# Performance work log

Measured on AMD Instinct MI355X. Metric: run time of the kernel, lower is better.

## Reference

```python
import jax, jax.numpy as jnp
import numpy as np

C_S, C_Z, MAX_LEN, N_AA, L = 256, 128, 1024, 21, 512
LN_EPS = 1e-5


def setup_inputs() -> dict:
    key = jax.random.key(0)
    ks = jax.random.split(key, 12)
    inp = {
        "seq": jax.random.randint(ks[0], (L,), 0, N_AA),
        "chain_id_res": jax.random.randint(ks[1], (L,), 0, 2),
        "res_idx": jax.random.randint(ks[2], (L,), 0, L),
        # learned parameters
        "E_aa": jax.random.normal(ks[3], (N_AA, C_S), jnp.float32) * 0.02,
        "E_pos": jax.random.normal(ks[4], (MAX_LEN, C_S), jnp.float32) * 0.02,
        "E_chain": jax.random.normal(ks[5], (2, C_S), jnp.float32) * 0.02,
        "E_chainpair": jax.random.normal(ks[6], (4, C_Z), jnp.float32) * 0.02,
        "E_relpos": jax.random.normal(ks[7], (66, C_Z), jnp.float32) * 0.02,
        "W_pair": jax.random.normal(ks[8], (3 * C_S, C_Z), jnp.float32) / np.sqrt(3 * C_S),
        "b_pair": jnp.zeros((C_Z,), jnp.float32),
        "ln_w": jnp.ones((C_S,), jnp.float32),
        "ln_b": jnp.zeros((C_S,), jnp.float32),
    }
    return inp


def reference(seq, chain_id_res, res_idx, E_aa, E_pos, E_chain, E_chainpair,
              E_relpos, W_pair, b_pair, ln_w, ln_b):
    # single rep: sum of three embedding lookups -> [L, c_s]
    s = E_aa[seq] + E_pos[res_idx] + E_chain[chain_id_res]

    # LayerNorm over last dim
    mu = jnp.mean(s, axis=-1, keepdims=True)
    var = jnp.mean(jnp.square(s - mu), axis=-1, keepdims=True)
    u = (s - mu) * jax.lax.rsqrt(var + LN_EPS) * ln_w + ln_b  # [L, c_s]

    # pair_proj(cat(u_i, u_j, u_i*u_j)) decomposed: W = [W1; W2; W3]
    W1, W2, W3 = W_pair[:C_S], W_pair[C_S:2 * C_S], W_pair[2 * C_S:]
    zi = u @ W1                                   # [L, c_z] per-i term
    zj = u @ W2                                   # [L, c_z] per-j term
    zx = jnp.einsum('ic,jc,cz->ijz', u, u, W3)    # cross term (u_i*u_j) @ W3
    z = zi[:, None, :] + zj[None, :, :] + zx + b_pair  # [L, L, c_z]

    # chain-pair and relative-position embeddings
    chain_pair = chain_id_res[:, None] * 2 + chain_id_res[None, :]  # [L, L] in [0,3]
    same_chain = chain_id_res[:, None] == chain_id_res[None, :]
    diff = res_idx[:, None] - res_idx[None, :]
    clipped = jnp.clip(diff, -32, 32) + 32
    relpos = jnp.where(same_chain, clipped, 65)  # cross-chain bucket = 65

    z = z + E_chainpair[chain_pair] + E_relpos[relpos]
    return s, z
```

## Files before the change

kernel.cpp:

```cpp
#include <hip/hip_runtime.h>
#include <hip/hip_bf16.h>

#define L 512
#define CS 256
#define CZ 128
#define LN_EPS 1e-5f

typedef _Float16 f16_t;
typedef f16_t f16x8 __attribute__((ext_vector_type(8)));
typedef float f32x4 __attribute__((ext_vector_type(4)));

__global__ __launch_bounds__(256) void k_prep(
    const int* __restrict__ seq, const int* __restrict__ cid,
    const int* __restrict__ ridx,
    const float* __restrict__ Eaa, const float* __restrict__ Epos,
    const float* __restrict__ Ech, const float* __restrict__ lnw,
    const float* __restrict__ lnb, const float* __restrict__ Wp,
    const float* __restrict__ bp, const float* __restrict__ Ecp,
    const float* __restrict__ Erp,
    float* __restrict__ s_out, f16_t* __restrict__ u2,
    float* __restrict__ zrow, float* __restrict__ zcol,
    f16_t* __restrict__ w3c, float* __restrict__ tab)
{
    __shared__ float su[CS];
    __shared__ float red[8];
    const int i = blockIdx.x;
    const int c = threadIdx.x;

    if (i < 128) {
        w3c[(c >> 3) * (CZ * 8) + i * 8 + (c & 7)] = (f16_t)Wp[(2 * CS + c) * CZ + i];
    } else if (i < 128 + 264) {
        const int b2 = i - 128;
        if (c < CZ)
            tab[b2 * CZ + c] = Ecp[(b2 / 66) * CZ + c] + Erp[(b2 % 66) * CZ + c];
    }

    const int sq = seq[i], ri = ridx[i], ci = cid[i];
    const float v = Eaa[sq * CS + c] + Epos[ri * CS + c] + Ech[ci * CS + c];
    s_out[i * CS + c] = v;

    float s1 = v, s2 = v * v;
    #pragma unroll
    for (int o = 32; o > 0; o >>= 1) {
        s1 += __shfl_down(s1, o, 64);
        s2 += __shfl_down(s2, o, 64);
    }
    const int wv = c >> 6, lane = c & 63;
    if (lane == 0) { red[wv * 2] = s1; red[wv * 2 + 1] = s2; }
    __syncthreads();
    const float S  = red[0] + red[2] + red[4] + red[6];
    const float SS = red[1] + red[3] + red[5] + red[7];
    const float mu  = S * (1.0f / CS);
    const float var = SS * (1.0f / CS) - mu * mu;
    const float rs  = rsqrtf(var + LN_EPS);
    const float u   = (v - mu) * rs * lnw[c] + lnb[c];
    u2[(c >> 3) * (L * 8) + i * 8 + (c & 7)] = (f16_t)u;
    su[c] = u;
    __syncthreads();

    const int z = c & 127;
    const int half = c >> 7;
    const float* W = Wp + half * CS * CZ + z;
    float a0 = 0, a1 = 0, a2 = 0, a3 = 0;
    #pragma unroll 8
    for (int cc = 0; cc < CS; cc += 4) {
        a0 += su[cc + 0] * W[(cc + 0) * CZ];
        a1 += su[cc + 1] * W[(cc + 1) * CZ];
        a2 += su[cc + 2] * W[(cc + 2) * CZ];
        a3 += su[cc + 3] * W[(cc + 3) * CZ];
    }
    const float acc = (a0 + a1) + (a2 + a3);
    if (half) zcol[i * CZ + z] = acc;
    else      zrow[i * CZ + z] = acc + bp[z];
}

__global__ __launch_bounds__(512, 4) void k_pair(
    const f16_t* __restrict__ u2, const f16_t* __restrict__ w3c,
    const float* __restrict__ zrow, const float* __restrict__ zcol,
    const float* __restrict__ tab,
    const int* __restrict__ cid, const int* __restrict__ ridx,
    float* __restrict__ zout)
{
    __shared__ f16_t lds[(1024 + 256) * 8];
    f16x8* lj = (f16x8*)lds;
    f16x8* li = ((f16x8*)lds) + 1024;

    const int t = threadIdx.x;
    const int lane = t & 63, wave = t >> 6;
    const int m = lane & 15, q = lane >> 4;
    const int j0 = blockIdx.x * 32, i0 = blockIdx.y * 8;
    const int zseg = wave * 16;
    const int zq = zseg + q * 4;

    const f16x8* pu = (const f16x8*)u2;
    const f16x8* pw = (const f16x8*)w3c;

    if (t < 256) li[t] = pu[(t >> 3) * L + i0 + (t & 7)];
    #pragma unroll
    for (int rep = 0; rep < 2; ++rep) {
        const int un = rep * 512 + t;
        lj[un] = pu[(un >> 5) * L + j0 + (un & 31)];
    }

    f16x8 A[8];
    #pragma unroll
    for (int k32 = 0; k32 < 8; ++k32)
        A[k32] = pw[(k32 * 4 + q) * CZ + zseg + m];

    const int ja = j0 + m, jb = j0 + 16 + m;
    const int cja = cid[ja], rja = ridx[ja];
    const int cjb = cid[jb], rjb = ridx[jb];
    f32x4 ZCa = *(const f32x4*)&zcol[ja * CZ + zq];
    f32x4 ZCb = *(const f32x4*)&zcol[jb * CZ + zq];

    __syncthreads();

    #pragma unroll
    for (int ig = 0; ig < 4; ++ig) {
        const int i_0 = i0 + ig * 2, i_1 = i_0 + 1;

        const int ci0 = cid[i_0], ri0 = ridx[i_0];
        const int ci1 = cid[i_1], ri1 = ridx[i_1];
        int d;
        d = ri0 - rja; d = d < -32 ? -32 : (d > 32 ? 32 : d);
        const int x0a = ((ci0 * 2 + cja) * 66) + ((ci0 == cja) ? (d + 32) : 65);
        d = ri0 - rjb; d = d < -32 ? -32 : (d > 32 ? 32 : d);
        const int x0b = ((ci0 * 2 + cjb) * 66) + ((ci0 == cjb) ? (d + 32) : 65);
        d = ri1 - rja; d = d < -32 ? -32 : (d > 32 ? 32 : d);
        const int x1a = ((ci1 * 2 + cja) * 66) + ((ci1 == cja) ? (d + 32) : 65);
        d = ri1 - rjb; d = d < -32 ? -32 : (d > 32 ? 32 : d);
        const int x1b = ((ci1 * 2 + cjb) * 66) + ((ci1 == cjb) ? (d + 32) : 65);
        f32x4 zr0 = *(const f32x4*)&zrow[i_0 * CZ + zq];
        f32x4 zr1 = *(const f32x4*)&zrow[i_1 * CZ + zq];
        f32x4 t0a = *(const f32x4*)&tab[x0a * CZ + zq];
        f32x4 t0b = *(const f32x4*)&tab[x0b * CZ + zq];
        f32x4 t1a = *(const f32x4*)&tab[x1a * CZ + zq];
        f32x4 t1b = *(const f32x4*)&tab[x1b * CZ + zq];

        f32x4 a0a = {0,0,0,0}, a0b = {0,0,0,0};
        f32x4 a1a = {0,0,0,0}, a1b = {0,0,0,0};
        #pragma unroll
        for (int k32 = 0; k32 < 8; ++k32) {
            const int cb = k32 * 4 + q;
            f16x8 uja = lj[cb * 32 + m];
            f16x8 ujb = lj[cb * 32 + 16 + m];
            f16x8 ui0 = li[cb * 8 + ig * 2];
            f16x8 ui1 = li[cb * 8 + ig * 2 + 1];
            a0a = __builtin_amdgcn_mfma_f32_16x16x32_f16(A[k32], ui0 * uja, a0a, 0, 0, 0);
            a0b = __builtin_amdgcn_mfma_f32_16x16x32_f16(A[k32], ui0 * ujb, a0b, 0, 0, 0);
            a1a = __builtin_amdgcn_mfma_f32_16x16x32_f16(A[k32], ui1 * uja, a1a, 0, 0, 0);
            a1b = __builtin_amdgcn_mfma_f32_16x16x32_f16(A[k32], ui1 * ujb, a1b, 0, 0, 0);
        }

        float* r0 = zout + ((size_t)i_0 * L + j0 + m) * CZ + zq;
        float* r1 = zout + ((size_t)i_1 * L + j0 + m) * CZ + zq;
        f32x4 o;
        o = a0a + zr0 + ZCa + t0a; *(f32x4*)r0 = o;
        o = a0b + zr0 + ZCb + t0b; *(f32x4*)(r0 + 16 * CZ) = o;
        o = a1a + zr1 + ZCa + t1a; *(f32x4*)r1 = o;
        o = a1b + zr1 + ZCb + t1b; *(f32x4*)(r1 + 16 * CZ) = o;
    }
}

extern "C" void kernel_launch(void* const* d_in, const int* in_sizes, int n_in,
                              void* d_out, int out_size, void* d_ws, size_t ws_size,
                              hipStream_t stream) {
    const int*   seq  = (const int*)d_in[0];
    const int*   cid  = (const int*)d_in[1];
    const int*   ridx = (const int*)d_in[2];
    const float* Eaa  = (const float*)d_in[3];
    const float* Epos = (const float*)d_in[4];
    const float* Ech  = (const float*)d_in[5];
    const float* Ecp  = (const float*)d_in[6];
    const float* Erp  = (const float*)d_in[7];
    const float* Wp   = (const float*)d_in[8];
    const float* bp   = (const float*)d_in[9];
    const float* lnw  = (const float*)d_in[10];
    const float* lnb  = (const float*)d_in[11];

    float* out   = (float*)d_out;
    float* s_out = out;
    float* zout  = out + L * CS;

    char* ws = (char*)d_ws;
    f16_t* u2   = (f16_t*)ws;
    f16_t* w3c  = (f16_t*)(ws + 262144);
    float* zrow = (float*)(ws + 327680);
    float* zcol = (float*)(ws + 589824);
    float* tab  = (float*)(ws + 851968);

    hipLaunchKernelGGL(k_prep, dim3(L), dim3(256), 0, stream,
                       seq, cid, ridx, Eaa, Epos, Ech, lnw, lnb, Wp, bp,
                       Ecp, Erp, s_out, u2, zrow, zcol, w3c, tab);
    hipLaunchKernelGGL(k_pair, dim3(16, 64), dim3(512), 0, stream,
                       u2, w3c, zrow, zcol, tab, cid, ridx, zout);
}
```

Baseline: 173.0 us.

## Drop LDS staging in pair kernel and retile waves over z and i

Removes the shared-memory staging and the block barrier from the pair kernel. Each wave now loads its u_j fragments, two W3 fragments and per-i u vectors straight from global memory into registers. Blocks cover 16 j by 8 i, and each wave handles 32 z channels for 4 i rows, so the grid doubles along j. Occupancy launch bounds drop from 4 to 2 to allow more registers per thread. In exchange, global load traffic per block rises and fewer waves are resident, which could hurt latency hiding in a kernel dominated by output stores.

```diff
diff --git a/kernel.cpp b/kernel.cpp
--- a/kernel.cpp
+++ b/kernel.cpp
@@ -74,91 +74,84 @@
     else      zrow[i * CZ + z] = acc + bp[z];
 }
 
-__global__ __launch_bounds__(512, 4) void k_pair(
+__global__ __launch_bounds__(512, 2) void k_pair(
     const f16_t* __restrict__ u2, const f16_t* __restrict__ w3c,
     const float* __restrict__ zrow, const float* __restrict__ zcol,
     const float* __restrict__ tab,
     const int* __restrict__ cid, const int* __restrict__ ridx,
     float* __restrict__ zout)
 {
-    __shared__ f16_t lds[(1024 + 256) * 8];
-    f16x8* lj = (f16x8*)lds;
-    f16x8* li = ((f16x8*)lds) + 1024;
-
     const int t = threadIdx.x;
     const int lane = t & 63, wave = t >> 6;
     const int m = lane & 15, q = lane >> 4;
-    const int j0 = blockIdx.x * 32, i0 = blockIdx.y * 8;
-    const int zseg = wave * 16;
-    const int zq = zseg + q * 4;
+    const int j0 = blockIdx.x * 16, i0 = blockIdx.y * 8;
+    const int zsg = (wave & 3) * 32;
+    const int ibase = i0 + (wave >> 2) * 4;
+    const int zq0 = zsg + q * 4;
+    const int zq1 = zsg + 16 + q * 4;
 
     const f16x8* pu = (const f16x8*)u2;
     const f16x8* pw = (const f16x8*)w3c;
 
-    if (t < 256) li[t] = pu[(t >> 3) * L + i0 + (t & 7)];
+    f16x8 A0[8], A1[8], Uj[8];
     #pragma unroll
-    for (int rep = 0; rep < 2; ++rep) {
-        const int un = rep * 512 + t;
-        lj[un] = pu[(un >> 5) * L + j0 + (un & 31)];
+    for (int k32 = 0; k32 < 8; ++k32) {
+        const int cb = k32 * 4 + q;
+        A0[k32] = pw[cb * CZ + zsg + m];
+        A1[k32] = pw[cb * CZ + zsg + 16 + m];
+        Uj[k32] = pu[cb * L + j0 + m];
     }
+    const int jm = j0 + m;
+    const int cj = cid[jm], rj = ridx[jm];
+    const f32x4 ZC0 = *(const f32x4*)&zcol[jm * CZ + zq0];
+    const f32x4 ZC1 = *(const f32x4*)&zcol[jm * CZ + zq1];
 
-    f16x8 A[8];
-    #pragma unroll
-    for (int k32 = 0; k32 < 8; ++k32)
-        A[k32] = pw[(k32 * 4 + q) * CZ + zseg + m];
+    for (int ip = 0; ip < 2; ++ip) {
+        const int ia = ibase + ip * 2, ib = ia + 1;
 
-    const int ja = j0 + m, jb = j0 + 16 + m;
-    const int cja = cid[ja], rja = ridx[ja];
-    const int cjb = cid[jb], rjb = ridx[jb];
-    f32x4 ZCa = *(const f32x4*)&zcol[ja * CZ + zq];
-    f32x4 ZCb = *(const f32x4*)&zcol[jb * CZ + zq];
-
-    __syncthreads();
-
-    #pragma unroll
-    for (int ig = 0; ig < 4; ++ig) {
-        const int i_0 = i0 + ig * 2, i_1 = i_0 + 1;
-
-        const int ci0 = cid[i_0], ri0 = ridx[i_0];
-        const int ci1 = cid[i_1], ri1 = ridx[i_1];
-        int d;
-        d = ri0 - rja; d = d < -32 ? -32 : (d > 32 ? 32 : d);
-        const int x0a = ((ci0 * 2 + cja) * 66) + ((ci0 == cja) ? (d + 32) : 65);
-        d = ri0 - rjb; d = d < -32 ? -32 : (d > 32 ? 32 : d);
-        const int x0b = ((ci0 * 2 + cjb) * 66) + ((ci0 == cjb) ? (d + 32) : 65);
-        d = ri1 - rja; d = d < -32 ? -32 : (d > 32 ? 32 : d);
-        const int x1a = ((ci1 * 2 + cja) * 66) + ((ci1 == cja) ? (d + 32) : 65);
-        d = ri1 - rjb; d = d < -32 ? -32 : (d > 32 ? 32 : d);
-        const int x1b = ((ci1 * 2 + cjb) * 66) + ((ci1 == cjb) ? (d + 32) : 65);
-        f32x4 zr0 = *(const f32x4*)&zrow[i_0 * CZ + zq];
-        f32x4 zr1 = *(const f32x4*)&zrow[i_1 * CZ + zq];
-        f32x4 t0a = *(const f32x4*)&tab[x0a * CZ + zq];
-        f32x4 t0b = *(const f32x4*)&tab[x0b * CZ + zq];
-        f32x4 t1a = *(const f32x4*)&tab[x1a * CZ + zq];
-        f32x4 t1b = *(const f32x4*)&tab[x1b * CZ + zq];
-
-        f32x4 a0a = {0,0,0,0}, a0b = {0,0,0,0};
-        f32x4 a1a = {0,0,0,0}, a1b = {0,0,0,0};
+        f16x8 Ua[8], Ub[8];
         #pragma unroll
         for (int k32 = 0; k32 < 8; ++k32) {
             const int cb = k32 * 4 + q;
-            f16x8 uja = lj[cb * 32 + m];
-            f16x8 ujb = lj[cb * 32 + 16 + m];
-            f16x8 ui0 = li[cb * 8 + ig * 2];
-            f16x8 ui1 = li[cb * 8 + ig * 2 + 1];
-            a0a = __builtin_amdgcn_mfma_f32_16x16x32_f16(A[k32], ui0 * uja, a0a, 0, 0, 0);
-            a0b = __builtin_amdgcn_mfma_f32_16x16x32_f16(A[k32], ui0 * ujb, a0b, 0, 0, 0);
-            a1a = __builtin_amdgcn_mfma_f32_16x16x32_f16(A[k32], ui1 * uja, a1a, 0, 0, 0);
-            a1b = __builtin_amdgcn_mfma_f32_16x16x32_f16(A[k32], ui1 * ujb, a1b, 0, 0, 0);
+            Ua[k32] = pu[cb * L + ia];
+            Ub[k32] = pu[cb * L + ib];
         }
 
-        float* r0 = zout + ((size_t)i_0 * L + j0 + m) * CZ + zq;
-        float* r1 = zout + ((size_t)i_1 * L + j0 + m) * CZ + zq;
+        const int ca = cid[ia], ra = ridx[ia];
+        const int cb2 = cid[ib], rb2 = ridx[ib];
+        int d;
+        d = ra - rj;  d = d < -32 ? -32 : (d > 32 ? 32 : d);
+        const int xa = ((ca * 2 + cj) * 66) + ((ca == cj) ? (d + 32) : 65);
+        d = rb2 - rj; d = d < -32 ? -32 : (d > 32 ? 32 : d);
+        const int xb = ((cb2 * 2 + cj) * 66) + ((cb2 == cj) ? (d + 32) : 65);
+        f32x4 zra0 = *(const f32x4*)&zrow[ia * CZ + zq0];
+        f32x4 zra1 = *(const f32x4*)&zrow[ia * CZ + zq1];
+        f32x4 zrb0 = *(const f32x4*)&zrow[ib * CZ + zq0];
+        f32x4 zrb1 = *(const f32x4*)&zrow[ib * CZ + zq1];
+        f32x4 ta0 = *(const f32x4*)&tab[xa * CZ + zq0];
+        f32x4 ta1 = *(const f32x4*)&tab[xa * CZ + zq1];
+        f32x4 tb0 = *(const f32x4*)&tab[xb * CZ + zq0];
+        f32x4 tb1 = *(const f32x4*)&tab[xb * CZ + zq1];
+
+        f32x4 aa0 = {0,0,0,0}, aa1 = {0,0,0,0};
+        f32x4 ab0 = {0,0,0,0}, ab1 = {0,0,0,0};
+        #pragma unroll
+        for (int k32 = 0; k32 < 8; ++k32) {
+            const f16x8 Ba = Ua[k32] * Uj[k32];
+            const f16x8 Bb = Ub[k32] * Uj[k32];
+            aa0 = __builtin_amdgcn_mfma_f32_16x16x32_f16(A0[k32], Ba, aa0, 0, 0, 0);
+            aa1 = __builtin_amdgcn_mfma_f32_16x16x32_f16(A1[k32], Ba, aa1, 0, 0, 0);
+            ab0 = __builtin_amdgcn_mfma_f32_16x16x32_f16(A0[k32], Bb, ab0, 0, 0, 0);
+            ab1 = __builtin_amdgcn_mfma_f32_16x16x32_f16(A1[k32], Bb, ab1, 0, 0, 0);
+        }
+
+        float* r_a = zout + ((size_t)ia * L + jm) * CZ;
+        float* r_b = zout + ((size_t)ib * L + jm) * CZ;
         f32x4 o;
-        o = a0a + zr0 + ZCa + t0a; *(f32x4*)r0 = o;
-        o = a0b + zr0 + ZCb + t0b; *(f32x4*)(r0 + 16 * CZ) = o;
-        o = a1a + zr1 + ZCa + t1a; *(f32x4*)r1 = o;
-        o = a1b + zr1 + ZCb + t1b; *(f32x4*)(r1 + 16 * CZ) = o;
+        o = aa0 + zra0 + ZC0 + ta0; *(f32x4*)(r_a + zq0) = o;
+        o = aa1 + zra1 + ZC1 + ta1; *(f32x4*)(r_a + zq1) = o;
+        o = ab0 + zrb0 + ZC0 + tb0; *(f32x4*)(r_b + zq0) = o;
+        o = ab1 + zrb1 + ZC1 + tb1; *(f32x4*)(r_b + zq1) = o;
     }
 }
 
@@ -192,6 +185,6 @@
     hipLaunchKernelGGL(k_prep, dim3(L), dim3(256), 0, stream,
                        seq, cid, ridx, Eaa, Epos, Ech, lnw, lnb, Wp, bp,
                        Ecp, Erp, s_out, u2, zrow, zcol, w3c, tab);
-    hipLaunchKernelGGL(k_pair, dim3(16, 64), dim3(512), 0, stream,
+    hipLaunchKernelGGL(k_pair, dim3(32, 64), dim3(512), 0, stream,
                        u2, w3c, zrow, zcol, tab, cid, ridx, zout);
 }
```

Measured after the change: 219.4 us. +26.8%, slower.

## Retile pair kernel waves over (j-half, i-half, z-half) with 4x4 MFMA register tiles

Applied to the files above, without the earlier changes.

Each wave now covers 16 j × 4 i × 64 z instead of 32 j × 8 i × 16 z. The W3 fragments are loaded per k-step from global memory rather than held in registers for the whole kernel. Each product vector u_i*u_j is reused across 4 z-tiles, which cuts the elementwise multiplies and LDS reads per MFMA. All MFMAs are issued before a single epilogue. Launch bounds drop to 2 blocks per SM to fit the 16 accumulators, which trades occupancy for register tiling.

```diff
diff --git a/kernel.cpp b/kernel.cpp
--- a/kernel.cpp
+++ b/kernel.cpp
@@ -74,7 +74,7 @@
     else      zrow[i * CZ + z] = acc + bp[z];
 }
 
-__global__ __launch_bounds__(512, 4) void k_pair(
+__global__ __launch_bounds__(512, 2) void k_pair(
     const f16_t* __restrict__ u2, const f16_t* __restrict__ w3c,
     const float* __restrict__ zrow, const float* __restrict__ zcol,
     const float* __restrict__ tab,
@@ -89,8 +89,12 @@
     const int lane = t & 63, wave = t >> 6;
     const int m = lane & 15, q = lane >> 4;
     const int j0 = blockIdx.x * 32, i0 = blockIdx.y * 8;
-    const int zseg = wave * 16;
-    const int zq = zseg + q * 4;
+    const int jh = wave & 1;
+    const int ih = (wave >> 1) & 1;
+    const int zh = wave >> 2;
+    const int jm = j0 + jh * 16 + m;
+    const int ib = ih * 4;
+    const int zb = zh * 64;
 
     const f16x8* pu = (const f16x8*)u2;
     const f16x8* pw = (const f16x8*)w3c;
@@ -101,64 +105,54 @@
         const int un = rep * 512 + t;
         lj[un] = pu[(un >> 5) * L + j0 + (un & 31)];
     }
-
-    f16x8 A[8];
-    #pragma unroll
-    for (int k32 = 0; k32 < 8; ++k32)
-        A[k32] = pw[(k32 * 4 + q) * CZ + zseg + m];
-
-    const int ja = j0 + m, jb = j0 + 16 + m;
-    const int cja = cid[ja], rja = ridx[ja];
-    const int cjb = cid[jb], rjb = ridx[jb];
-    f32x4 ZCa = *(const f32x4*)&zcol[ja * CZ + zq];
-    f32x4 ZCb = *(const f32x4*)&zcol[jb * CZ + zq];
-
     __syncthreads();
 
+    f32x4 acc[4][4];
     #pragma unroll
-    for (int ig = 0; ig < 4; ++ig) {
-        const int i_0 = i0 + ig * 2, i_1 = i_0 + 1;
+    for (int ii = 0; ii < 4; ++ii)
+        #pragma unroll
+        for (int zt = 0; zt < 4; ++zt)
+            acc[ii][zt] = (f32x4){0.f, 0.f, 0.f, 0.f};
 
-        const int ci0 = cid[i_0], ri0 = ridx[i_0];
-        const int ci1 = cid[i_1], ri1 = ridx[i_1];
-        int d;
-        d = ri0 - rja; d = d < -32 ? -32 : (d > 32 ? 32 : d);
-        const int x0a = ((ci0 * 2 + cja) * 66) + ((ci0 == cja) ? (d + 32) : 65);
-        d = ri0 - rjb; d = d < -32 ? -32 : (d > 32 ? 32 : d);
-        const int x0b = ((ci0 * 2 + cjb) * 66) + ((ci0 == cjb) ? (d + 32) : 65);
-        d = ri1 - rja; d = d < -32 ? -32 : (d > 32 ? 32 : d);
-        const int x1a = ((ci1 * 2 + cja) * 66) + ((ci1 == cja) ? (d + 32) : 65);
-        d = ri1 - rjb; d = d < -32 ? -32 : (d > 32 ? 32 : d);
-        const int x1b = ((ci1 * 2 + cjb) * 66) + ((ci1 == cjb) ? (d + 32) : 65);
-        f32x4 zr0 = *(const f32x4*)&zrow[i_0 * CZ + zq];
-        f32x4 zr1 = *(const f32x4*)&zrow[i_1 * CZ + zq];
-        f32x4 t0a = *(const f32x4*)&tab[x0a * CZ + zq];
-        f32x4 t0b = *(const f32x4*)&tab[x0b * CZ + zq];
-        f32x4 t1a = *(const f32x4*)&tab[x1a * CZ + zq];
-        f32x4 t1b = *(const f32x4*)&tab[x1b * CZ + zq];
+    #pragma unroll
+    for (int k32 = 0; k32 < 8; ++k32) {
+        const int cb = k32 * 4 + q;
+        f16x8 Az[4];
+        #pragma unroll
+        for (int zt = 0; zt < 4; ++zt)
+            Az[zt] = pw[cb * CZ + zb + zt * 16 + m];
+        const f16x8 ujv = lj[cb * 32 + jh * 16 + m];
+        #pragma unroll
+        for (int ii = 0; ii < 4; ++ii) {
+            const f16x8 B = li[cb * 8 + ib + ii] * ujv;
+            #pragma unroll
+            for (int zt = 0; zt < 4; ++zt)
+                acc[ii][zt] = __builtin_amdgcn_mfma_f32_16x16x32_f16(
+                    Az[zt], B, acc[ii][zt], 0, 0, 0);
+        }
+    }
 
-        f32x4 a0a = {0,0,0,0}, a0b = {0,0,0,0};
-        f32x4 a1a = {0,0,0,0}, a1b = {0,0,0,0};
+    const int cj = cid[jm], rj = ridx[jm];
+    f32x4 ZC[4];
+    #pragma unroll
+    for (int zt = 0; zt < 4; ++zt)
+        ZC[zt] = *(const f32x4*)&zcol[jm * CZ + zb + zt * 16 + q * 4];
+
+    #pragma unroll
+    for (int ii = 0; ii < 4; ++ii) {
+        const int i = i0 + ib + ii;
+        const int ci = cid[i], ri = ridx[i];
+        int d = ri - rj; d = d < -32 ? -32 : (d > 32 ? 32 : d);
+        const int x = ((ci * 2 + cj) * 66) + ((ci == cj) ? (d + 32) : 65);
+        float* r_o = zout + ((size_t)i * L + jm) * CZ;
         #pragma unroll
-        for (int k32 = 0; k32 < 8; ++k32) {
-            const int cb = k32 * 4 + q;
-            f16x8 uja = lj[cb * 32 + m];
-            f16x8 ujb = lj[cb * 32 + 16 + m];
-            f16x8 ui0 = li[cb * 8 + ig * 2];
-            f16x8 ui1 = li[cb * 8 + ig * 2 + 1];
-            a0a = __builtin_amdgcn_mfma_f32_16x16x32_f16(A[k32], ui0 * uja, a0a, 0, 0, 0);
-            a0b = __builtin_amdgcn_mfma_f32_16x16x32_f16(A[k32], ui0 * ujb, a0b, 0, 0, 0);
-            a1a = __builtin_amdgcn_mfma_f32_16x16x32_f16(A[k32], ui1 * uja, a1a, 0, 0, 0);
-            a1b = __builtin_amdgcn_mfma_f32_16x16x32_f16(A[k32], ui1 * ujb, a1b, 0, 0, 0);
+        for (int zt = 0; zt < 4; ++zt) {
+            const int zo = zb + zt * 16 + q * 4;
+            const f32x4 zr = *(const f32x4*)&zrow[i * CZ + zo];
+            const f32x4 tb = *(const f32x4*)&tab[x * CZ + zo];
+            const f32x4 o = acc[ii][zt] + zr + ZC[zt] + tb;
+            *(f32x4*)(r_o + zo) = o;
         }
-
-        float* r0 = zout + ((size_t)i_0 * L + j0 + m) * CZ + zq;
-        float* r1 = zout + ((size_t)i_1 * L + j0 + m) * CZ + zq;
-        f32x4 o;
-        o = a0a + zr0 + ZCa + t0a; *(f32x4*)r0 = o;
-        o = a0b + zr0 + ZCb + t0b; *(f32x4*)(r0 + 16 * CZ) = o;
-        o = a1a + zr1 + ZCa + t1a; *(f32x4*)r1 = o;
-        o = a1b + zr1 + ZCb + t1b; *(f32x4*)(r1 + 16 * CZ) = o;
     }
 }
 
```

Result: slower. 193.8 us (+12.0%).
